# Optimization experiments

Measured on AMD Instinct MI355X. Metric: run time of the kernel, lower is better.

Reference implementation:

```python
import jax, jax.numpy as jnp
import numpy as np

# dims
M, C, D = 64, 2000, 512          # clients, classes, embed_dim
H = 4                             # num_heads
HD = D // H                       # head_dim = 128
DFF = 2048                        # torch TransformerEncoderLayer default dim_feedforward
NUM_CLASSES = 2000
EPS = 1e-5


def _ln(x, g, b):
    mu = jnp.mean(x, axis=-1, keepdims=True)
    var = jnp.mean(jnp.square(x - mu), axis=-1, keepdims=True)
    return (x - mu) * jax.lax.rsqrt(var + EPS) * g + b


def setup_inputs() -> dict:
    key = jax.random.key(0)
    ks = jax.random.split(key, 16)
    s = 0.02
    return {
        "client_protos": jax.random.normal(ks[0], (M, C, D), jnp.float32),
        "norm_g": jnp.ones((D,), jnp.float32),
        "norm_b": jnp.zeros((D,), jnp.float32),
        "in_proj_w": jax.random.normal(ks[1], (3 * D, D), jnp.float32) * s,
        "in_proj_b": jnp.zeros((3 * D,), jnp.float32),
        "out_proj_w": jax.random.normal(ks[2], (D, D), jnp.float32) * s,
        "out_proj_b": jnp.zeros((D,), jnp.float32),
        "lin1_w": jax.random.normal(ks[3], (DFF, D), jnp.float32) * s,
        "lin1_b": jnp.zeros((DFF,), jnp.float32),
        "lin2_w": jax.random.normal(ks[4], (D, DFF), jnp.float32) * s,
        "lin2_b": jnp.zeros((D,), jnp.float32),
        "norm1_g": jnp.ones((D,), jnp.float32),
        "norm1_b": jnp.zeros((D,), jnp.float32),
        "norm2_g": jnp.ones((D,), jnp.float32),
        "norm2_b": jnp.zeros((D,), jnp.float32),
        "global_query": jax.random.normal(ks[5], (NUM_CLASSES, D), jnp.float32),
        "all_labels": jax.random.randint(ks[6], (C,), 0, NUM_CLASSES, jnp.int32),
        "round_num": 10,
        "client_idx": 0,
    }


def reference(client_protos, norm_g, norm_b, in_proj_w, in_proj_b,
              out_proj_w, out_proj_b, lin1_w, lin1_b, lin2_w, lin2_b,
              norm1_g, norm1_b, norm2_g, norm2_b, global_query,
              all_labels, round_num, client_idx):
    # 1) LayerNorm over all prototypes: (M, C, D)
    x = _ln(client_protos, norm_g, norm_b)
    # 2) Per-class transformer: original loops c in range(C) on (1, M, D).
    #    Batched: treat C as batch -> (C, M, D). Post-norm torch encoder layer.
    x = jnp.transpose(x, (1, 0, 2))  # (C, M, D)
    # self-attention
    qkv = x @ in_proj_w.T + in_proj_b          # (C, M, 3D)
    q, k, v = jnp.split(qkv, 3, axis=-1)
    q = q.reshape(C, M, H, HD)
    k = k.reshape(C, M, H, HD)
    v = v.reshape(C, M, H, HD)
    scores = jnp.einsum('cqhd,ckhd->chqk', q, k) / np.sqrt(HD).astype(np.float32)
    attn = jax.nn.softmax(scores, axis=-1)
    sa = jnp.einsum('chqk,ckhd->cqhd', attn, v).reshape(C, M, D)
    sa = sa @ out_proj_w.T + out_proj_b
    x = _ln(x + sa, norm1_g, norm1_b)
    # feed-forward (relu, dropout = eval no-op)
    ff = jax.nn.relu(x @ lin1_w.T + lin1_b) @ lin2_w.T + lin2_b
    x = _ln(x + ff, norm2_g, norm2_b)           # (C, M, D) == protos_trans^T
    # 3) Cross-attention with per-class global query
    q_all = global_query[all_labels].reshape(C, H, HD)
    kv_all = x.reshape(C, M, H, HD)
    s2 = jnp.einsum('chd,cmhd->chm', q_all, kv_all) / np.sqrt(HD).astype(np.float32)
    w2 = jax.nn.softmax(s2, axis=-1)
    attn_out = jnp.einsum('chm,cmhd->chd', w2, kv_all).reshape(C, D)
    return attn_out
```

## Files before the change

kernel.cpp:

```cpp
#include <hip/hip_runtime.h>

typedef _Float16 f16;
typedef _Float16 half8 __attribute__((ext_vector_type(8)));
typedef float f32x4 __attribute__((ext_vector_type(4)));

typedef __attribute__((address_space(1))) void* as1v;
typedef __attribute__((address_space(3))) void* as3v;

#define SCALE 0.08838834764831845f

static __device__ __forceinline__ f32x4 mfma16(half8 a, half8 b, f32x4 c){
  return __builtin_amdgcn_mfma_f32_16x16x32_f16(a, b, c, 0, 0, 0);
}

__global__ __launch_bounds__(256) void k_cvt(const float* __restrict__ src, f16* __restrict__ dst, int n){
  int i = (blockIdx.x * 256 + threadIdx.x) * 8;
  if (i >= n) return;
  float4 a = *(const float4*)(src + i);
  float4 b = *(const float4*)(src + i + 4);
  half8 h;
  h[0] = (f16)a.x; h[1] = (f16)a.y; h[2] = (f16)a.z; h[3] = (f16)a.w;
  h[4] = (f16)b.x; h[5] = (f16)b.y; h[6] = (f16)b.z; h[7] = (f16)b.w;
  *(half8*)(dst + i) = h;
}

__global__ __launch_bounds__(256) void k_ln0(const float* __restrict__ protos,
                                             const float* __restrict__ g,
                                             const float* __restrict__ bb,
                                             f16* __restrict__ xb, int c0){
  const int w = threadIdx.x >> 6, l = threadIdx.x & 63;
  const int q = blockIdx.x * 4 + w;
  const int cl = q >> 6, m = q & 63;
  const float* in = protos + ((size_t)m * 2000 + (size_t)(c0 + cl)) * 512;
  const int d0 = l * 8;
  float4 a = *(const float4*)(in + d0);
  float4 c = *(const float4*)(in + d0 + 4);
  float s  = a.x + a.y + a.z + a.w + c.x + c.y + c.z + c.w;
  float ss = a.x*a.x + a.y*a.y + a.z*a.z + a.w*a.w + c.x*c.x + c.y*c.y + c.z*c.z + c.w*c.w;
#pragma unroll
  for (int msk = 1; msk < 64; msk <<= 1){ s += __shfl_xor(s, msk); ss += __shfl_xor(ss, msk); }
  const float mu = s * (1.f/512.f);
  const float rs = rsqrtf(ss * (1.f/512.f) - mu*mu + 1e-5f);
  float4 g0 = *(const float4*)(g + d0),  g1 = *(const float4*)(g + d0 + 4);
  float4 b0 = *(const float4*)(bb + d0), b1 = *(const float4*)(bb + d0 + 4);
  half8 o;
  o[0] = (f16)((a.x - mu) * rs * g0.x + b0.x);
  o[1] = (f16)((a.y - mu) * rs * g0.y + b0.y);
  o[2] = (f16)((a.z - mu) * rs * g0.z + b0.z);
  o[3] = (f16)((a.w - mu) * rs * g0.w + b0.w);
  o[4] = (f16)((c.x - mu) * rs * g1.x + b1.x);
  o[5] = (f16)((c.y - mu) * rs * g1.y + b1.y);
  o[6] = (f16)((c.z - mu) * rs * g1.z + b1.z);
  o[7] = (f16)((c.w - mu) * rs * g1.w + b1.w);
  *(half8*)(xb + (size_t)q * 512 + d0) = o;
}

__global__ __launch_bounds__(256) void k_resln(const float* __restrict__ t, const f16* __restrict__ skip,
                                               const float* __restrict__ g, const float* __restrict__ bb,
                                               f16* __restrict__ outp){
  const int w = threadIdx.x >> 6, l = threadIdx.x & 63;
  const size_t q = (size_t)blockIdx.x * 4 + w;
  const int d0 = l * 8;
  const float* tin = t + q * 512 + d0;
  half8 sk = *(const half8*)(skip + q * 512 + d0);
  float4 a = *(const float4*)tin;
  float4 c = *(const float4*)(tin + 4);
  float v0 = a.x + (float)sk[0], v1 = a.y + (float)sk[1], v2 = a.z + (float)sk[2], v3 = a.w + (float)sk[3];
  float v4 = c.x + (float)sk[4], v5 = c.y + (float)sk[5], v6 = c.z + (float)sk[6], v7 = c.w + (float)sk[7];
  float s  = v0+v1+v2+v3+v4+v5+v6+v7;
  float ss = v0*v0+v1*v1+v2*v2+v3*v3+v4*v4+v5*v5+v6*v6+v7*v7;
#pragma unroll
  for (int msk = 1; msk < 64; msk <<= 1){ s += __shfl_xor(s, msk); ss += __shfl_xor(ss, msk); }
  const float mu = s * (1.f/512.f);
  const float rs = rsqrtf(ss * (1.f/512.f) - mu*mu + 1e-5f);
  float4 g0 = *(const float4*)(g + d0),  g1 = *(const float4*)(g + d0 + 4);
  float4 b0 = *(const float4*)(bb + d0), b1 = *(const float4*)(bb + d0 + 4);
  half8 o;
  o[0] = (f16)((v0 - mu) * rs * g0.x + b0.x);
  o[1] = (f16)((v1 - mu) * rs * g0.y + b0.y);
  o[2] = (f16)((v2 - mu) * rs * g0.z + b0.z);
  o[3] = (f16)((v3 - mu) * rs * g0.w + b0.w);
  o[4] = (f16)((v4 - mu) * rs * g1.x + b1.x);
  o[5] = (f16)((v5 - mu) * rs * g1.y + b1.y);
  o[6] = (f16)((v6 - mu) * rs * g1.z + b1.z);
  o[7] = (f16)((v7 - mu) * rs * g1.w + b1.w);
  *(half8*)(outp + q * 512 + d0) = o;
}

#define GLL(gp, lp) __builtin_amdgcn_global_load_lds((as1v)(void*)(gp), (as3v)(lp), 16, 0, 0)

template<bool RELU, bool OUTF32>
__global__ __launch_bounds__(512, 2) void k_gemm(const f16* __restrict__ A, const f16* __restrict__ B,
                                                 const float* __restrict__ bias, void* __restrict__ Cout,
                                                 int N, int K, int gn){
  extern __shared__ char smem_raw[];
  f16* sA = (f16*)smem_raw;
  f16* sB = sA + 4 * 8192;

  const int t = threadIdx.x, w = t >> 6, l = t & 63;
  const int wr = w >> 2, wc = w & 3;

  const int nwg = gridDim.x;
  const int q8 = nwg >> 3, r8 = nwg & 7;
  const int xcd = blockIdx.x & 7, lidx = blockIdx.x >> 3;
  const int swz = (xcd < r8 ? xcd * (q8 + 1) : r8 * (q8 + 1) + (xcd - r8) * q8) + lidx;
  const int tm = swz / gn, tn = swz % gn;
  const size_t row0 = (size_t)tm * 256;
  const int col0 = tn * 256;

  f32x4 acc[8][4];
#pragma unroll
  for (int m = 0; m < 8; ++m)
#pragma unroll
    for (int n = 0; n < 4; ++n) acc[m][n] = (f32x4){0.f,0.f,0.f,0.f};

  const int swcol = ((l & 3) ^ ((l >> 3) & 3)) * 8;
  const size_t ga0 = (row0 + (size_t)(w * 32 + (l >> 2))) * (size_t)K + swcol;
  const size_t ga1 = ga0 + (size_t)16 * K;
  const size_t gb0 = ((size_t)col0 + (size_t)(w * 32 + (l >> 2))) * (size_t)K + swcol;
  const size_t gb1 = gb0 + (size_t)16 * K;
  const int lw0 = (w * 2 + 0) * 512;
  const int lw1 = (w * 2 + 1) * 512;

  const int rdbase = (l & 15) * 32 + (((l >> 4) ^ ((l >> 1) & 3)) << 3);
  const int abase = wr * 4096 + rdbase;
  const int bbase = wc * 2048 + rdbase;

  const int NT = K >> 5;

#pragma unroll
  for (int tp = 0; tp < 3; ++tp){
    GLL(A + ga0 + tp * 32, sA + tp * 8192 + lw0);
    GLL(A + ga1 + tp * 32, sA + tp * 8192 + lw1);
    GLL(B + gb0 + tp * 32, sB + tp * 8192 + lw0);
    GLL(B + gb1 + tp * 32, sB + tp * 8192 + lw1);
  }
  asm volatile("s_waitcnt vmcnt(8)" ::: "memory");
  __builtin_amdgcn_s_barrier();

  for (int tk = 0; tk < NT; ++tk){
    const f16* a_ = sA + (tk & 3) * 8192;
    const f16* b_ = sB + (tk & 3) * 8192;

    half8 bf[4], af[4];
#pragma unroll
    for (int n = 0; n < 4; ++n) bf[n] = *(const half8*)(b_ + bbase + n * 512);
#pragma unroll
    for (int m = 0; m < 4; ++m) af[m] = *(const half8*)(a_ + abase + m * 512);
    if (tk + 3 < NT){
      const int bb = (tk + 3) & 3; const size_t ko = (size_t)(tk + 3) * 32;
      GLL(A + ga0 + ko, sA + bb * 8192 + lw0);
      GLL(A + ga1 + ko, sA + bb * 8192 + lw1);
    }
    __builtin_amdgcn_s_barrier();
    asm volatile("s_waitcnt lgkmcnt(0)" ::: "memory");
    __builtin_amdgcn_sched_barrier(0);
    __builtin_amdgcn_s_setprio(1);
#pragma unroll
    for (int m = 0; m < 4; ++m)
#pragma unroll
      for (int n = 0; n < 4; ++n)
        acc[m][n] = mfma16(af[m], bf[n], acc[m][n]);
    __builtin_amdgcn_s_setprio(0);
    __builtin_amdgcn_s_barrier();

    half8 ag[4];
#pragma unroll
    for (int m = 0; m < 4; ++m) ag[m] = *(const half8*)(a_ + abase + 2048 + m * 512);
    if (tk + 3 < NT){
      const int bb = (tk + 3) & 3; const size_t ko = (size_t)(tk + 3) * 32;
      GLL(B + gb0 + ko, sB + bb * 8192 + lw0);
      GLL(B + gb1 + ko, sB + bb * 8192 + lw1);
    }
    __builtin_amdgcn_s_barrier();
    asm volatile("s_waitcnt lgkmcnt(0)" ::: "memory");
    __builtin_amdgcn_sched_barrier(0);
    __builtin_amdgcn_s_setprio(1);
#pragma unroll
    for (int m = 0; m < 4; ++m)
#pragma unroll
      for (int n = 0; n < 4; ++n)
        acc[m + 4][n] = mfma16(ag[m], bf[n], acc[m + 4][n]);
    __builtin_amdgcn_s_setprio(0);
    if (tk + 1 < NT){
      if (tk + 3 < NT)      { asm volatile("s_waitcnt vmcnt(8)" ::: "memory"); }
      else if (tk + 2 < NT) { asm volatile("s_waitcnt vmcnt(4)" ::: "memory"); }
      else                  { asm volatile("s_waitcnt vmcnt(0)" ::: "memory"); }
    }
    __builtin_amdgcn_s_barrier();
  }

#pragma unroll
  for (int m = 0; m < 8; ++m){
    const int r0 = wr * 128 + m * 16 + ((l >> 4) << 2);
#pragma unroll
    for (int n = 0; n < 4; ++n){
      const int c = col0 + wc * 64 + n * 16 + (l & 15);
      const float bs = bias[c];
#pragma unroll
      for (int j = 0; j < 4; ++j){
        float v = acc[m][n][j] + bs;
        if (RELU) v = fmaxf(v, 0.f);
        const size_t idx = (row0 + (size_t)(r0 + j)) * (size_t)N + (size_t)c;
        if (OUTF32) ((float*)Cout)[idx] = v;
        else        ((f16*)Cout)[idx] = (f16)v;
      }
    }
  }
}

__global__ __launch_bounds__(256) void k_attn(const f16* __restrict__ qkv, f16* __restrict__ sa){
  __shared__ __align__(16) f16 P[4][4096];
  __shared__ __align__(16) f16 VT[4][4096];
  const int cl = blockIdx.x;
  const int h = threadIdx.x >> 6, l = threadIdx.x & 63;
  const f16* base = qkv + (size_t)cl * 64 * 1536;
  const f16* Qp = base + h * 128;
  const f16* Kp = base + 512 + h * 128;
  const f16* Vp = base + 1024 + h * 128;

  f32x4 s[4][4];
#pragma unroll
  for (int x = 0; x < 4; ++x)
#pragma unroll
    for (int y = 0; y < 4; ++y) s[x][y] = (f32x4){0.f,0.f,0.f,0.f};
#pragma unroll
  for (int ks = 0; ks < 4; ++ks){
    half8 aq[4], bk[4];
#pragma unroll
    for (int x = 0; x < 4; ++x)
      aq[x] = *(const half8*)&Qp[(size_t)(x * 16 + (l & 15)) * 1536 + ks * 32 + (l >> 4) * 8];
#pragma unroll
    for (int y = 0; y < 4; ++y)
      bk[y] = *(const half8*)&Kp[(size_t)(y * 16 + (l & 15)) * 1536 + ks * 32 + (l >> 4) * 8];
#pragma unroll
    for (int x = 0; x < 4; ++x)
#pragma unroll
      for (int y = 0; y < 4; ++y)
        s[x][y] = mfma16(aq[x], bk[y], s[x][y]);
  }

  char* Pb = (char*)&P[h][0];
#pragma unroll
  for (int x = 0; x < 4; ++x){
#pragma unroll
    for (int j = 0; j < 4; ++j){
      float e0 = s[x][0][j] * SCALE;
      float e1 = s[x][1][j] * SCALE;
      float e2 = s[x][2][j] * SCALE;
      float e3 = s[x][3][j] * SCALE;
      float mx = fmaxf(fmaxf(e0, e1), fmaxf(e2, e3));
#pragma unroll
      for (int msk = 1; msk < 16; msk <<= 1) mx = fmaxf(mx, __shfl_xor(mx, msk));
      e0 = __expf(e0 - mx); e1 = __expf(e1 - mx); e2 = __expf(e2 - mx); e3 = __expf(e3 - mx);
      float sm = e0 + e1 + e2 + e3;
#pragma unroll
      for (int msk = 1; msk < 16; msk <<= 1) sm += __shfl_xor(sm, msk);
      const float inv = 1.f / sm;
      const int row = x * 16 + (l >> 4) * 4 + j;
      const int rb = row * 128 + (l & 15) * 2;
      const int rsw = (row & 7) << 4;
      *(f16*)(Pb + ((rb     ) ^ rsw)) = (f16)(e0 * inv);
      *(f16*)(Pb + ((rb + 32) ^ rsw)) = (f16)(e1 * inv);
      *(f16*)(Pb + ((rb + 64) ^ rsw)) = (f16)(e2 * inv);
      *(f16*)(Pb + ((rb + 96) ^ rsw)) = (f16)(e3 * inv);
    }
  }

  char* Vb = (char*)&VT[h][0];
#pragma unroll
  for (int dh = 0; dh < 2; ++dh){
#pragma unroll
    for (int it = 0; it < 8; ++it){
      const int chunk = it * 64 + l;
      const int m = chunk >> 3, dc = chunk & 7;
      half8 v = *(const half8*)&Vp[(size_t)m * 1536 + dh * 64 + dc * 8];
#pragma unroll
      for (int jj = 0; jj < 8; ++jj){
        const int dd = dc * 8 + jj;
        *(f16*)(Vb + ((dd * 128 + m * 2) ^ ((dd & 7) << 4))) = v[jj];
      }
    }
    __syncthreads();
#pragma unroll
    for (int x = 0; x < 4; ++x){
      const int ar = x * 16 + (l & 15);
      const int ab = ar * 128, sw = (ar & 7) << 4;
      half8 ap0 = *(const half8*)(Pb + ((ab + (l >> 4) * 16) ^ sw));
      half8 ap1 = *(const half8*)(Pb + ((ab + 64 + (l >> 4) * 16) ^ sw));
#pragma unroll
      for (int dt = 0; dt < 4; ++dt){
        const int vr = dt * 16 + (l & 15);
        const int vb = vr * 128, vsw = (vr & 7) << 4;
        half8 b0 = *(const half8*)(Vb + ((vb + (l >> 4) * 16) ^ vsw));
        half8 b1 = *(const half8*)(Vb + ((vb + 64 + (l >> 4) * 16) ^ vsw));
        f32x4 o = (f32x4){0.f,0.f,0.f,0.f};
        o = mfma16(ap0, b0, o);
        o = mfma16(ap1, b1, o);
#pragma unroll
        for (int j = 0; j < 4; ++j){
          const int mrow = x * 16 + (l >> 4) * 4 + j;
          const int dcol = dh * 64 + dt * 16 + (l & 15);
          sa[((size_t)cl * 64 + mrow) * 512 + h * 128 + dcol] = (f16)o[j];
        }
      }
    }
    __syncthreads();
  }
}

__global__ __launch_bounds__(256) void k_cross(const f16* __restrict__ z, const float* __restrict__ gq,
                                               const int* __restrict__ labels, float* __restrict__ out,
                                               int c0){
  const int cl = blockIdx.x;
  const int h = threadIdx.x >> 6, l = threadIdx.x & 63;
  const int cg = c0 + cl;
  const float* q = gq + (size_t)labels[cg] * 512 + h * 128;
  const f16* zb = z + (size_t)cl * 64 * 512 + h * 128;

  const f16* zr = zb + (size_t)l * 512;
  float s = 0.f;
#pragma unroll
  for (int d = 0; d < 128; d += 8){
    half8 v = *(const half8*)&zr[d];
    float4 q0 = *(const float4*)&q[d];
    float4 q1 = *(const float4*)&q[d + 4];
    s += q0.x*(float)v[0] + q0.y*(float)v[1] + q0.z*(float)v[2] + q0.w*(float)v[3]
       + q1.x*(float)v[4] + q1.y*(float)v[5] + q1.z*(float)v[6] + q1.w*(float)v[7];
  }
  s *= SCALE;
  float mx = s;
#pragma unroll
  for (int msk = 1; msk < 64; msk <<= 1) mx = fmaxf(mx, __shfl_xor(mx, msk));
  float e = __expf(s - mx);
  float sm = e;
#pragma unroll
  for (int msk = 1; msk < 64; msk <<= 1) sm += __shfl_xor(sm, msk);
  const float wgt = e / sm;

  float a0 = 0.f, a1 = 0.f;
  for (int m = 0; m < 64; ++m){
    const float wm = __shfl(wgt, m);
    const f16* zm = zb + (size_t)m * 512 + 2 * l;
    a0 += wm * (float)zm[0];
    a1 += wm * (float)zm[1];
  }
  float2 o; o.x = a0; o.y = a1;
  *(float2*)&out[(size_t)cg * 512 + h * 128 + 2 * l] = o;
}

extern "C" void kernel_launch(void* const* d_in, const int* in_sizes, int n_in,
                              void* d_out, int out_size, void* d_ws, size_t ws_size,
                              hipStream_t stream){
  (void)in_sizes; (void)n_in; (void)out_size;
  const float* protos = (const float*)d_in[0];
  const float* norm_g = (const float*)d_in[1];
  const float* norm_b = (const float*)d_in[2];
  const float* in_w   = (const float*)d_in[3];
  const float* in_b   = (const float*)d_in[4];
  const float* ow     = (const float*)d_in[5];
  const float* ob     = (const float*)d_in[6];
  const float* l1w    = (const float*)d_in[7];
  const float* l1b    = (const float*)d_in[8];
  const float* l2w    = (const float*)d_in[9];
  const float* l2b    = (const float*)d_in[10];
  const float* n1g    = (const float*)d_in[11];
  const float* n1b    = (const float*)d_in[12];
  const float* n2g    = (const float*)d_in[13];
  const float* n2b    = (const float*)d_in[14];
  const float* gq     = (const float*)d_in[15];
  const int*   labels = (const int*)d_in[16];
  float* out = (float*)d_out;

  char* p = (char*)d_ws;
  auto alloc = [&](size_t bytes)->char*{
    char* r = p; p += (bytes + 255) & ~(size_t)255; return r;
  };
  f16* Wq = (f16*)alloc((size_t)1536*512*2);
  f16* Wo = (f16*)alloc((size_t)512*512*2);
  f16* W1 = (f16*)alloc((size_t)2048*512*2);
  f16* W2 = (f16*)alloc((size_t)512*2048*2);
  const size_t fixed = (size_t)(p - (char*)d_ws);

  const size_t per_class = (size_t)64*512*2 + (size_t)64*2048*2 + (size_t)64*512*2 + (size_t)64*512*4;
  long long avail = (long long)ws_size - (long long)fixed - 8192;
  long long cc_max = avail > 0 ? avail / (long long)per_class : 0;
  int Cc = (int)(cc_max > 2000 ? 2000 : cc_max);
  Cc &= ~3;
  if (Cc < 4) Cc = 4;

  f16*   xb  = (f16*)  alloc((size_t)Cc*64*512*2);
  f16*   big = (f16*)  alloc((size_t)Cc*64*2048*2);
  f16*   sac = (f16*)  alloc((size_t)Cc*64*512*2);
  float* tmp = (float*)alloc((size_t)Cc*64*512*4);

  k_cvt<<<1536*512/2048, 256, 0, stream>>>(in_w, Wq, 1536*512);
  k_cvt<<<512*512/2048,  256, 0, stream>>>(ow,   Wo, 512*512);
  k_cvt<<<2048*512/2048, 256, 0, stream>>>(l1w,  W1, 2048*512);
  k_cvt<<<2048*512/2048, 256, 0, stream>>>(l2w,  W2, 512*2048);

  const size_t SMEM = 131072;
  for (int c0 = 0; c0 < 2000; c0 += Cc){
    const int cc = (2000 - c0 < Cc) ? (2000 - c0) : Cc;
    const int R = cc * 64;
    const int gm = R / 256;
    k_ln0<<<R/4, 256, 0, stream>>>(protos, norm_g, norm_b, xb, c0);
    k_gemm<false,false><<<gm*6, 512, SMEM, stream>>>(xb, Wq, in_b, big, 1536, 512, 6);
    k_attn<<<cc, 256, 0, stream>>>(big, sac);
    k_gemm<false,true><<<gm*2, 512, SMEM, stream>>>(sac, Wo, ob, tmp, 512, 512, 2);
    k_resln<<<R/4, 256, 0, stream>>>(tmp, xb, n1g, n1b, sac);
    k_gemm<true,false><<<gm*8, 512, SMEM, stream>>>(sac, W1, l1b, big, 2048, 512, 8);
    k_gemm<false,true><<<gm*2, 512, SMEM, stream>>>(big, W2, l2b, tmp, 512, 2048, 2);
    k_resln<<<R/4, 256, 0, stream>>>(tmp, sac, n2g, n2b, big);
    k_cross<<<cc, 256, 0, stream>>>(big, gq, labels, out, c0);
  }
}
```

Measured before the change: 1.698 ms.

## Restructure GEMM main loop to BK=64 double-buffered tiles with swapped MFMA operands

The GEMM K-loop changes from a 4-stage ring of 32-wide K tiles to a 2-stage double buffer of 64-wide K tiles with a new 8-way XOR swizzle. Each loop iteration now covers twice the K and needs fewer barriers. The MFMA operands are swapped so each lane ends up holding four consecutive output columns, which allows vectorised float4/half4 stores and a float4 bias load in the epilogue. The cost is a shallower prefetch: the loop waits for all outstanding loads (vmcnt(0)) every iteration, which could expose global load latency.

New measurement: 1.708 ms. No clear change (+0.6%).

```diff
diff --git a/kernel.cpp b/kernel.cpp
--- a/kernel.cpp
+++ b/kernel.cpp
@@ -1,6 +1,7 @@
 #include <hip/hip_runtime.h>
 
 typedef _Float16 f16;
+typedef _Float16 half4 __attribute__((ext_vector_type(4)));
 typedef _Float16 half8 __attribute__((ext_vector_type(8)));
 typedef float f32x4 __attribute__((ext_vector_type(4)));
 
@@ -95,7 +96,7 @@
                                                  int N, int K, int gn){
   extern __shared__ char smem_raw[];
   f16* sA = (f16*)smem_raw;
-  f16* sB = sA + 4 * 8192;
+  f16* sB = sA + 2 * 16384;
 
   const int t = threadIdx.x, w = t >> 6, l = t & 63;
   const int wr = w >> 2, wc = w & 3;
@@ -114,96 +115,109 @@
 #pragma unroll
     for (int n = 0; n < 4; ++n) acc[m][n] = (f32x4){0.f,0.f,0.f,0.f};
 
-  const int swcol = ((l & 3) ^ ((l >> 3) & 3)) * 8;
-  const size_t ga0 = (row0 + (size_t)(w * 32 + (l >> 2))) * (size_t)K + swcol;
-  const size_t ga1 = ga0 + (size_t)16 * K;
-  const size_t gb0 = ((size_t)col0 + (size_t)(w * 32 + (l >> 2))) * (size_t)K + swcol;
-  const size_t gb1 = gb0 + (size_t)16 * K;
-  const int lw0 = (w * 2 + 0) * 512;
-  const int lw1 = (w * 2 + 1) * 512;
-
-  const int rdbase = (l & 15) * 32 + (((l >> 4) ^ ((l >> 1) & 3)) << 3);
-  const int abase = wr * 4096 + rdbase;
-  const int bbase = wc * 2048 + rdbase;
-
-  const int NT = K >> 5;
-
-#pragma unroll
-  for (int tp = 0; tp < 3; ++tp){
-    GLL(A + ga0 + tp * 32, sA + tp * 8192 + lw0);
-    GLL(A + ga1 + tp * 32, sA + tp * 8192 + lw1);
-    GLL(B + gb0 + tp * 32, sB + tp * 8192 + lw0);
-    GLL(B + gb1 + tp * 32, sB + tp * 8192 + lw1);
-  }
-  asm volatile("s_waitcnt vmcnt(8)" ::: "memory");
+  const int rl0 = w * 32 + (l >> 3);
+  const int csw = (((l & 7) ^ ((l >> 3) & 7))) * 8;
+  const f16* gA = A + (row0 + (size_t)rl0) * (size_t)K + csw;
+  const f16* gB = B + ((size_t)col0 + (size_t)rl0) * (size_t)K + csw;
+  const int ldst = w * 4 * 512;
+
+  const int rbase = (l & 15) * 64;
+  const int sl0 = ((((0 << 2) + (l >> 4)) ^ (l & 7)) << 3);
+  const int sl1 = ((((1 << 2) + (l >> 4)) ^ (l & 7)) << 3);
+
+  const int NT = K >> 6;
+
+#pragma unroll
+  for (int i = 0; i < 4; ++i){
+    GLL(gA + (size_t)i * 8 * K, sA + ldst + i * 512);
+    GLL(gB + (size_t)i * 8 * K, sB + ldst + i * 512);
+  }
+  asm volatile("s_waitcnt vmcnt(0)" ::: "memory");
   __builtin_amdgcn_s_barrier();
 
   for (int tk = 0; tk < NT; ++tk){
-    const f16* a_ = sA + (tk & 3) * 8192;
-    const f16* b_ = sB + (tk & 3) * 8192;
-
-    half8 bf[4], af[4];
-#pragma unroll
-    for (int n = 0; n < 4; ++n) bf[n] = *(const half8*)(b_ + bbase + n * 512);
-#pragma unroll
-    for (int m = 0; m < 4; ++m) af[m] = *(const half8*)(a_ + abase + m * 512);
-    if (tk + 3 < NT){
-      const int bb = (tk + 3) & 3; const size_t ko = (size_t)(tk + 3) * 32;
-      GLL(A + ga0 + ko, sA + bb * 8192 + lw0);
-      GLL(A + ga1 + ko, sA + bb * 8192 + lw1);
-    }
-    __builtin_amdgcn_s_barrier();
+    const f16* a_ = sA + (tk & 1) * 16384;
+    const f16* b_ = sB + (tk & 1) * 16384;
+    const int nb = ((tk + 1) & 1) * 16384;
+    const bool more = (tk + 1) < NT;
+
+    if (more){
+      const size_t ko = (size_t)(tk + 1) * 64;
+#pragma unroll
+      for (int i = 0; i < 4; ++i)
+        GLL(gA + (size_t)i * 8 * K + ko, sA + nb + ldst + i * 512);
+    }
+    half8 bf[4][2], af[4][2];
+#pragma unroll
+    for (int n = 0; n < 4; ++n){
+      bf[n][0] = *(const half8*)(b_ + wc * 4096 + n * 1024 + rbase + sl0);
+      bf[n][1] = *(const half8*)(b_ + wc * 4096 + n * 1024 + rbase + sl1);
+    }
+#pragma unroll
+    for (int m = 0; m < 4; ++m){
+      af[m][0] = *(const half8*)(a_ + wr * 8192 + m * 1024 + rbase + sl0);
+      af[m][1] = *(const half8*)(a_ + wr * 8192 + m * 1024 + rbase + sl1);
+    }
     asm volatile("s_waitcnt lgkmcnt(0)" ::: "memory");
     __builtin_amdgcn_sched_barrier(0);
     __builtin_amdgcn_s_setprio(1);
 #pragma unroll
-    for (int m = 0; m < 4; ++m)
-#pragma unroll
-      for (int n = 0; n < 4; ++n)
-        acc[m][n] = mfma16(af[m], bf[n], acc[m][n]);
+    for (int ks = 0; ks < 2; ++ks)
+#pragma unroll
+      for (int m = 0; m < 4; ++m)
+#pragma unroll
+        for (int n = 0; n < 4; ++n)
+          acc[m][n] = mfma16(bf[n][ks], af[m][ks], acc[m][n]);
     __builtin_amdgcn_s_setprio(0);
-    __builtin_amdgcn_s_barrier();
-
-    half8 ag[4];
-#pragma unroll
-    for (int m = 0; m < 4; ++m) ag[m] = *(const half8*)(a_ + abase + 2048 + m * 512);
-    if (tk + 3 < NT){
-      const int bb = (tk + 3) & 3; const size_t ko = (size_t)(tk + 3) * 32;
-      GLL(B + gb0 + ko, sB + bb * 8192 + lw0);
-      GLL(B + gb1 + ko, sB + bb * 8192 + lw1);
-    }
-    __builtin_amdgcn_s_barrier();
+
+    if (more){
+      const size_t ko = (size_t)(tk + 1) * 64;
+#pragma unroll
+      for (int i = 0; i < 4; ++i)
+        GLL(gB + (size_t)i * 8 * K + ko, sB + nb + ldst + i * 512);
+    }
+    half8 ag[4][2];
+#pragma unroll
+    for (int m = 0; m < 4; ++m){
+      ag[m][0] = *(const half8*)(a_ + wr * 8192 + 4096 + m * 1024 + rbase + sl0);
+      ag[m][1] = *(const half8*)(a_ + wr * 8192 + 4096 + m * 1024 + rbase + sl1);
+    }
     asm volatile("s_waitcnt lgkmcnt(0)" ::: "memory");
     __builtin_amdgcn_sched_barrier(0);
     __builtin_amdgcn_s_setprio(1);
 #pragma unroll
-    for (int m = 0; m < 4; ++m)
-#pragma unroll
-      for (int n = 0; n < 4; ++n)
-        acc[m + 4][n] = mfma16(ag[m], bf[n], acc[m + 4][n]);
+    for (int ks = 0; ks < 2; ++ks)
+#pragma unroll
+      for (int m = 0; m < 4; ++m)
+#pragma unroll
+        for (int n = 0; n < 4; ++n)
+          acc[m + 4][n] = mfma16(bf[n][ks], ag[m][ks], acc[m + 4][n]);
     __builtin_amdgcn_s_setprio(0);
-    if (tk + 1 < NT){
-      if (tk + 3 < NT)      { asm volatile("s_waitcnt vmcnt(8)" ::: "memory"); }
-      else if (tk + 2 < NT) { asm volatile("s_waitcnt vmcnt(4)" ::: "memory"); }
-      else                  { asm volatile("s_waitcnt vmcnt(0)" ::: "memory"); }
-    }
+    asm volatile("s_waitcnt vmcnt(0)" ::: "memory");
     __builtin_amdgcn_s_barrier();
   }
 
+  float4 bias4[4];
+#pragma unroll
+  for (int n = 0; n < 4; ++n)
+    bias4[n] = *(const float4*)(bias + col0 + wc * 64 + n * 16 + ((l >> 4) << 2));
 #pragma unroll
   for (int m = 0; m < 8; ++m){
-    const int r0 = wr * 128 + m * 16 + ((l >> 4) << 2);
+    const size_t r = row0 + (size_t)(wr * 128 + m * 16 + (l & 15));
 #pragma unroll
     for (int n = 0; n < 4; ++n){
-      const int c = col0 + wc * 64 + n * 16 + (l & 15);
-      const float bs = bias[c];
-#pragma unroll
-      for (int j = 0; j < 4; ++j){
-        float v = acc[m][n][j] + bs;
-        if (RELU) v = fmaxf(v, 0.f);
-        const size_t idx = (row0 + (size_t)(r0 + j)) * (size_t)N + (size_t)c;
-        if (OUTF32) ((float*)Cout)[idx] = v;
-        else        ((f16*)Cout)[idx] = (f16)v;
+      const int c = col0 + wc * 64 + n * 16 + ((l >> 4) << 2);
+      float v0 = acc[m][n][0] + bias4[n].x;
+      float v1 = acc[m][n][1] + bias4[n].y;
+      float v2 = acc[m][n][2] + bias4[n].z;
+      float v3 = acc[m][n][3] + bias4[n].w;
+      if (RELU){ v0 = fmaxf(v0, 0.f); v1 = fmaxf(v1, 0.f); v2 = fmaxf(v2, 0.f); v3 = fmaxf(v3, 0.f); }
+      if (OUTF32){
+        float4 o; o.x = v0; o.y = v1; o.z = v2; o.w = v3;
+        *(float4*)&((float*)Cout)[r * (size_t)N + c] = o;
+      } else {
+        half4 h; h[0] = (f16)v0; h[1] = (f16)v1; h[2] = (f16)v2; h[3] = (f16)v3;
+        *(half4*)&((f16*)Cout)[r * (size_t)N + c] = h;
       }
     }
   }
```
